# Performance work log

Measured on AMD Instinct MI355X. Metric: run time of the kernel, lower is better.

## Reference

```python
import jax, jax.numpy as jnp
import numpy as np

N_NODES = 100000
N_EDGES = 1600000
IN_CH, HID_CH, OUT_CH = 128, 128, 64
N_GRAPHS = 64


def gcn_conv(x, src, dst, W, b, n_nodes):
    """PyG-style GCNConv: self-loops already included in (src, dst).
    out_i = b + sum_j norm_ij * (x_j @ W), norm_ij = deg_i^-1/2 * deg_j^-1/2."""
    xw = x @ W  # [N, out]
    deg = jax.ops.segment_sum(jnp.ones_like(dst, dtype=xw.dtype), dst,
                              num_segments=n_nodes)  # [N]
    dinv = jnp.where(deg > 0, jax.lax.rsqrt(jnp.maximum(deg, 1e-12)), 0.0)
    norm = dinv[src] * dinv[dst]  # [E]
    msg = xw[src] * norm[:, None]  # gather + scale  [E, out]
    out = jax.ops.segment_sum(msg, dst, num_segments=n_nodes)  # scatter-add
    return out + b


def global_mean_pool(x, batch, n_graphs):
    s = jax.ops.segment_sum(x, batch, num_segments=n_graphs)
    cnt = jax.ops.segment_sum(jnp.ones((x.shape[0],), x.dtype), batch,
                              num_segments=n_graphs)
    return s / jnp.maximum(cnt, 1.0)[:, None]


def setup_inputs() -> dict:
    key = jax.random.key(0)
    ks = jax.random.split(key, 9)
    x = jax.random.normal(ks[0], (N_NODES, IN_CH), dtype=jnp.float32)
    edge_index = jax.random.randint(ks[1], (2, N_EDGES), 0, N_NODES, dtype=jnp.int64)
    batch = jnp.sort(jax.random.randint(ks[2], (N_NODES,), 0, N_GRAPHS, dtype=jnp.int64))
    # Glorot-ish params
    s1 = 1.0 / np.sqrt(IN_CH)
    s2 = 1.0 / np.sqrt(HID_CH)
    W1 = jax.random.normal(ks[3], (IN_CH, HID_CH), jnp.float32) * s1
    b1 = jnp.zeros((HID_CH,), jnp.float32)
    W2 = jax.random.normal(ks[4], (HID_CH, HID_CH), jnp.float32) * s2
    b2 = jnp.zeros((HID_CH,), jnp.float32)
    Wl = jax.random.normal(ks[5], (HID_CH, OUT_CH), jnp.float32) * s2
    bl = jax.random.normal(ks[6], (OUT_CH,), jnp.float32) * 0.01
    return {"x": x, "edge_index": edge_index, "batch": batch,
            "W1": W1, "b1": b1, "W2": W2, "b2": b2, "Wl": Wl, "bl": bl}


def reference(x, edge_index, batch, W1, b1, W2, b2, Wl, bl):
    n = x.shape[0]
    loop = jnp.arange(n, dtype=edge_index.dtype)
    src = jnp.concatenate([edge_index[0], loop])  # add self-loops
    dst = jnp.concatenate([edge_index[1], loop])
    h = jax.nn.relu(gcn_conv(x, src, dst, W1, b1, n))
    h = jax.nn.relu(gcn_conv(h, src, dst, W2, b2, n))
    g = global_mean_pool(h, batch, N_GRAPHS)  # [B, hid]
    return g @ Wl + bl  # [B, out]
```

## Files before the change

kernel.cpp:

```cpp
#include <hip/hip_runtime.h>

#define N_NODESC 100000
#define N_EDGESC 1600000
#define CH 128
#define NG 64
#define OC 64

#define GST_BLKS 391
#define EDGE_BLKS 6250
#define MFMA_BLKS 1563
#define NPASS 7
#define PAD_STRIDE 128

typedef __attribute__((ext_vector_type(8))) short short8;
typedef __attribute__((ext_vector_type(4))) float f32x4;

__device__ __forceinline__ unsigned short f2b_u(float f) {
    union { float f; unsigned int u; } x; x.f = f;
    unsigned int u = x.u;
    return (unsigned short)((u + 0x7fffu + ((u >> 16) & 1u)) >> 16);
}
__device__ __forceinline__ float b2f_lo(unsigned int v) {
    union { unsigned int u; float f; } x; x.u = v << 16; return x.f;
}
__device__ __forceinline__ float b2f_hi(unsigned int v) {
    union { unsigned int u; float f; } x; x.u = v & 0xffff0000u; return x.f;
}

#define WSTR 136
template<int AFP>
__device__ __forceinline__ void mfma_compute(int blk, int t, const void* __restrict__ Ap,
                                             unsigned short* __restrict__ Ob,
                                             const unsigned short* WsT) {
    int wave = t >> 6, lane = t & 63;
    int quad = lane >> 4, l16 = lane & 15;
    int arow = blk * 64 + wave * 16 + l16;
    bool rowok = arow < N_NODESC;
    f32x4 acc[8] = {};
#pragma unroll
    for (int c = 0; c < 4; ++c) {
        int koff = c * 32 + quad * 8;
        short8 a;
        if (AFP) {
            const float* A = (const float*)Ap;
            float4 f0 = make_float4(0, 0, 0, 0), f1 = make_float4(0, 0, 0, 0);
            if (rowok) {
                f0 = *(const float4*)(A + (size_t)arow * 128 + koff);
                f1 = *(const float4*)(A + (size_t)arow * 128 + koff + 4);
            }
            a[0] = (short)f2b_u(f0.x); a[1] = (short)f2b_u(f0.y);
            a[2] = (short)f2b_u(f0.z); a[3] = (short)f2b_u(f0.w);
            a[4] = (short)f2b_u(f1.x); a[5] = (short)f2b_u(f1.y);
            a[6] = (short)f2b_u(f1.z); a[7] = (short)f2b_u(f1.w);
        } else {
            const unsigned short* A = (const unsigned short*)Ap;
            if (rowok) a = *(const short8*)(A + (size_t)arow * 128 + koff);
            else       a = (short8)(short)0;
        }
#pragma unroll
        for (int tt = 0; tt < 8; ++tt) {
            short8 b = *(const short8*)&WsT[(tt * 16 + l16) * WSTR + koff];
            acc[tt] = __builtin_amdgcn_mfma_f32_16x16x32_bf16(a, b, acc[tt], 0, 0, 0);
        }
    }
    int orow0 = blk * 64 + wave * 16 + quad * 4;
#pragma unroll
    for (int r = 0; r < 4; ++r) {
        int g = orow0 + r;
        if (g < N_NODESC) {
#pragma unroll
            for (int tt = 0; tt < 8; ++tt)
                Ob[(size_t)g * 128 + tt * 16 + l16] = f2b_u(acc[tt][r]);
        }
    }
}

__global__ __launch_bounds__(256) void k_l1_build(const float* __restrict__ x,
                                                  const float* __restrict__ W1,
                                                  unsigned short* __restrict__ xw,
                                                  const int* __restrict__ ei,
                                                  int* __restrict__ deg,
                                                  int* __restrict__ pad) {
    __shared__ unsigned short WsT[128 * WSTR];
    int t = threadIdx.x;
    if (blockIdx.x < MFMA_BLKS) {
        for (int idx = t; idx < 16384; idx += 256) {
            int k = idx >> 7, c = idx & 127;
            WsT[c * WSTR + k] = f2b_u(W1[idx]);
        }
        __syncthreads();
        mfma_compute<1>(blockIdx.x, t, x, xw, WsT);
    } else {
        int bb = blockIdx.x - MFMA_BLKS;
        int e = (bb % EDGE_BLKS) * 256 + t;
        int p = bb / EDGE_BLKS;
        int d = ei[N_EDGESC + e];
        if ((d >> 14) == p) {
            int slot = atomicAdd(&deg[d], 1);
            pad[d * PAD_STRIDE + slot] = ei[e];
        }
    }
}

__global__ void k_mid(const int* __restrict__ deg, const int* __restrict__ batch,
                      const float* __restrict__ W2,
                      float* __restrict__ dinv, int* __restrict__ gstart,
                      unsigned short* __restrict__ Wt2) {
    int b = blockIdx.x, t = threadIdx.x;
    if (b < GST_BLKS) {
        int i = b * 256 + t;
        if (i < N_NODESC) dinv[i] = rsqrtf((float)(deg[i] + 1));
    } else if (b < 2 * GST_BLKS) {
        int i = (b - GST_BLKS) * 256 + t;
        if (i >= N_NODESC) return;
        int bb = batch[i];
        int bp = (i == 0) ? -1 : batch[i - 1];
        for (int g = bp + 1; g <= bb; ++g) gstart[g] = i;
        if (i == N_NODESC - 1)
            for (int g = bb + 1; g <= NG; ++g) gstart[g] = N_NODESC;
    } else {
        int i = (b - 2 * GST_BLKS) * 256 + t;
        int k = i >> 7, c = i & 127;
        Wt2[c * 128 + k] = f2b_u(W2[k * 128 + c]);
    }
}

__global__ __launch_bounds__(256) void k_mfma2(const unsigned short* __restrict__ A,
                                               const unsigned short* __restrict__ Wt,
                                               unsigned short* __restrict__ Ob) {
    __shared__ unsigned short WsT[128 * WSTR];
    int t = threadIdx.x;
    {
        const uint4* wsrc = (const uint4*)Wt;
        for (int idx = t; idx < 2048; idx += 256) {
            int row = idx >> 4, sub = idx & 15;
            *((uint4*)&WsT[row * WSTR] + sub) = wsrc[row * 16 + sub];
        }
    }
    __syncthreads();
    mfma_compute<0>(blockIdx.x, t, A, Ob, WsT);
}

__device__ __forceinline__ void gather_row(const unsigned int* __restrict__ xw,
                                           const int* __restrict__ pad,
                                           const float* __restrict__ dinv,
                                           int s, int e, int lane,
                                           float& acc0, float& acc1) {
    int i = s;
    for (; i + 8 <= e; i += 8) {
        int s0 = pad[i], s1 = pad[i + 1], s2 = pad[i + 2], s3 = pad[i + 3];
        int s4 = pad[i + 4], s5 = pad[i + 5], s6 = pad[i + 6], s7 = pad[i + 7];
        float w0 = dinv[s0], w1 = dinv[s1], w2 = dinv[s2], w3 = dinv[s3];
        float w4 = dinv[s4], w5 = dinv[s5], w6 = dinv[s6], w7 = dinv[s7];
        unsigned int v0 = xw[(size_t)s0 * 64 + lane];
        unsigned int v1 = xw[(size_t)s1 * 64 + lane];
        unsigned int v2 = xw[(size_t)s2 * 64 + lane];
        unsigned int v3 = xw[(size_t)s3 * 64 + lane];
        unsigned int v4 = xw[(size_t)s4 * 64 + lane];
        unsigned int v5 = xw[(size_t)s5 * 64 + lane];
        unsigned int v6 = xw[(size_t)s6 * 64 + lane];
        unsigned int v7 = xw[(size_t)s7 * 64 + lane];
        acc0 += w0 * b2f_lo(v0); acc1 += w0 * b2f_hi(v0);
        acc0 += w1 * b2f_lo(v1); acc1 += w1 * b2f_hi(v1);
        acc0 += w2 * b2f_lo(v2); acc1 += w2 * b2f_hi(v2);
        acc0 += w3 * b2f_lo(v3); acc1 += w3 * b2f_hi(v3);
        acc0 += w4 * b2f_lo(v4); acc1 += w4 * b2f_hi(v4);
        acc0 += w5 * b2f_lo(v5); acc1 += w5 * b2f_hi(v5);
        acc0 += w6 * b2f_lo(v6); acc1 += w6 * b2f_hi(v6);
        acc0 += w7 * b2f_lo(v7); acc1 += w7 * b2f_hi(v7);
    }
    for (; i + 4 <= e; i += 4) {
        int s0 = pad[i], s1 = pad[i + 1], s2 = pad[i + 2], s3 = pad[i + 3];
        float w0 = dinv[s0], w1 = dinv[s1], w2 = dinv[s2], w3 = dinv[s3];
        unsigned int v0 = xw[(size_t)s0 * 64 + lane];
        unsigned int v1 = xw[(size_t)s1 * 64 + lane];
        unsigned int v2 = xw[(size_t)s2 * 64 + lane];
        unsigned int v3 = xw[(size_t)s3 * 64 + lane];
        acc0 += w0 * b2f_lo(v0); acc1 += w0 * b2f_hi(v0);
        acc0 += w1 * b2f_lo(v1); acc1 += w1 * b2f_hi(v1);
        acc0 += w2 * b2f_lo(v2); acc1 += w2 * b2f_hi(v2);
        acc0 += w3 * b2f_lo(v3); acc1 += w3 * b2f_hi(v3);
    }
    for (; i < e; ++i) {
        int s0 = pad[i];
        float w0 = dinv[s0];
        unsigned int v0 = xw[(size_t)s0 * 64 + lane];
        acc0 += w0 * b2f_lo(v0); acc1 += w0 * b2f_hi(v0);
    }
}

__global__ __launch_bounds__(256) void k_gather1(const unsigned int* __restrict__ xw,
                                                 const int* __restrict__ deg,
                                                 const int* __restrict__ pad,
                                                 const float* __restrict__ dinv,
                                                 const float* __restrict__ bias,
                                                 unsigned int* __restrict__ outp) {
    int t = threadIdx.x;
    int lane = t & 63;
    int node = blockIdx.x * 4 + (t >> 6);
    if (node >= N_NODESC) return;
    int s = node * PAD_STRIDE, e = s + deg[node];
    float wn = dinv[node];
    unsigned int vs = xw[(size_t)node * 64 + lane];
    float acc0 = wn * b2f_lo(vs), acc1 = wn * b2f_hi(vs);
    gather_row(xw, pad, dinv, s, e, lane, acc0, acc1);
    float2 b = ((const float2*)bias)[lane];
    float o0 = fmaxf(b.x + wn * acc0, 0.f);
    float o1 = fmaxf(b.y + wn * acc1, 0.f);
    outp[(size_t)node * 64 + lane] =
        ((unsigned int)f2b_u(o1) << 16) | (unsigned int)f2b_u(o0);
}

__global__ __launch_bounds__(256) void k_gather_pool(const unsigned int* __restrict__ xw,
                                                     const int* __restrict__ deg,
                                                     const int* __restrict__ pad,
                                                     const float* __restrict__ dinv,
                                                     const float* __restrict__ bias,
                                                     const int* __restrict__ batch,
                                                     float* __restrict__ gpart) {
    __shared__ float lds[4 * 128];
    int t = threadIdx.x, w = t >> 6, lane = t & 63;
    int base = blockIdx.x * 16;
    bool fast = batch[base] == batch[base + 15];
    float2 bv = ((const float2*)bias)[lane];
    float sum0 = 0.f, sum1 = 0.f;
#pragma unroll 1
    for (int j = 0; j < 4; ++j) {
        int node = base + w * 4 + j;
        int s = node * PAD_STRIDE, e = s + deg[node];
        float wn = dinv[node];
        unsigned int vs = xw[(size_t)node * 64 + lane];
        float acc0 = wn * b2f_lo(vs), acc1 = wn * b2f_hi(vs);
        gather_row(xw, pad, dinv, s, e, lane, acc0, acc1);
        float o0 = fmaxf(bv.x + wn * acc0, 0.f);
        float o1 = fmaxf(bv.y + wn * acc1, 0.f);
        if (fast) {
            sum0 += o0; sum1 += o1;
        } else {
            int g = batch[node];
            atomicAdd(&gpart[g * 128 + lane * 2], o0);
            atomicAdd(&gpart[g * 128 + lane * 2 + 1], o1);
        }
    }
    if (fast) {
        lds[w * 128 + lane * 2] = sum0;
        lds[w * 128 + lane * 2 + 1] = sum1;
        __syncthreads();
        if (t < 128) {
            float v = lds[t] + lds[128 + t] + lds[256 + t] + lds[384 + t];
            atomicAdd(&gpart[batch[base] * 128 + t], v);
        }
    }
}

__global__ void k_final(const float* __restrict__ gpart, const int* __restrict__ gstart,
                        const float* __restrict__ Wl, const float* __restrict__ bl,
                        float* __restrict__ out) {
    __shared__ float gs[128];
    int b = blockIdx.x;
    int o = threadIdx.x;
    gs[o] = gpart[b * 128 + o];
    gs[o + 64] = gpart[b * 128 + 64 + o];
    __syncthreads();
    int cnt = gstart[b + 1] - gstart[b];
    float sc = 1.f / (float)(cnt > 0 ? cnt : 1);
    float sum = 0.f;
    for (int k = 0; k < 128; ++k) sum += gs[k] * Wl[k * 64 + o];
    out[b * 64 + o] = bl[o] + sc * sum;
}

extern "C" void kernel_launch(void* const* d_in, const int* in_sizes, int n_in,
                              void* d_out, int out_size, void* d_ws, size_t ws_size,
                              hipStream_t stream) {
    const float* x    = (const float*)d_in[0];
    const int*   ei   = (const int*)d_in[1];
    const int*   batch= (const int*)d_in[2];
    const float* W1   = (const float*)d_in[3];
    const float* b1   = (const float*)d_in[4];
    const float* W2   = (const float*)d_in[5];
    const float* b2   = (const float*)d_in[6];
    const float* Wl   = (const float*)d_in[7];
    const float* bl   = (const float*)d_in[8];
    float* out = (float*)d_out;

    char* ws = (char*)d_ws;
    unsigned short* xw_s = (unsigned short*)ws; ws += (size_t)N_NODESC * CH * 2;
    unsigned short* h_b  = (unsigned short*)ws; ws += (size_t)N_NODESC * CH * 2;
    unsigned short* Wt2 = (unsigned short*)ws; ws += (size_t)CH * CH * 2;
    int*   deg    = (int*)ws;   ws += (size_t)N_NODESC * 4;
    float* dinv   = (float*)ws; ws += (size_t)N_NODESC * 4;
    int*   pad    = (int*)ws;   ws += (size_t)N_NODESC * PAD_STRIDE * 4;
    int*   gstart = (int*)ws;   ws += (NG + 8) * 4;
    float* gpart  = (float*)ws; ws += (size_t)NG * CH * 4;

    hipMemsetAsync(deg, 0, (size_t)N_NODESC * 4, stream);
    hipMemsetAsync(gpart, 0, (size_t)NG * CH * 4, stream);

    k_l1_build<<<MFMA_BLKS + NPASS * EDGE_BLKS, 256, 0, stream>>>(x, W1, xw_s,
                                                                  ei, deg, pad);
    k_mid<<<2 * GST_BLKS + 64, 256, 0, stream>>>(deg, batch, W2, dinv, gstart, Wt2);

    k_gather1<<<(N_NODESC + 3) / 4, 256, 0, stream>>>((const unsigned int*)xw_s,
        deg, pad, dinv, b1, (unsigned int*)h_b);
    k_mfma2<<<MFMA_BLKS, 256, 0, stream>>>(h_b, Wt2, xw_s);
    k_gather_pool<<<N_NODESC / 16, 256, 0, stream>>>((const unsigned int*)xw_s,
        deg, pad, dinv, b2, batch, gpart);

    k_final<<<NG, 64, 0, stream>>>(gpart, gstart, Wl, bl, out);
}
```

Baseline: 349.5 us.

## Restructure CSR build into 8 range passes, fold dinv into gathers, merge memsets

The edge bucketing now uses 8 destination-range partitions, each block looping over 16 edge chunks, in place of 7 passes with one block per chunk. The build blocks are also placed before the MFMA blocks in the launch. The separate dinv kernel and array are removed, and rsqrt(deg+1) is recomputed inline in the gathers. W2 packing and gstart setup move to a small kernel ahead of the build, and the two memsets become one by making deg and gpart adjacent. This cuts a launch and a memset and reduces the blocks issued for edge scanning, but it adds an rsqrt per gathered edge and masks the slot index into the padded row.

```diff
diff --git a/kernel.cpp b/kernel.cpp
--- a/kernel.cpp
+++ b/kernel.cpp
@@ -9,8 +9,11 @@
 #define GST_BLKS 391
 #define EDGE_BLKS 6250
 #define MFMA_BLKS 1563
-#define NPASS 7
 #define PAD_STRIDE 128
+#define RANGE 12500
+#define EB_PER_BLK 16
+#define BGROUPS ((EDGE_BLKS + EB_PER_BLK - 1) / EB_PER_BLK)
+#define BUILD_BLKS (8 * BGROUPS)
 
 typedef __attribute__((ext_vector_type(8))) short short8;
 typedef __attribute__((ext_vector_type(4))) float f32x4;
@@ -25,6 +28,9 @@
 }
 __device__ __forceinline__ float b2f_hi(unsigned int v) {
     union { unsigned int u; float f; } x; x.u = v & 0xffff0000u; return x.f;
+}
+__device__ __forceinline__ float dinv_of(const int* __restrict__ deg, int i) {
+    return rsqrtf((float)(deg[i] + 1));
 }
 
 #define WSTR 136
@@ -75,6 +81,24 @@
     }
 }
 
+__global__ void k_pack(const float* __restrict__ W2, const int* __restrict__ batch,
+                       unsigned short* __restrict__ Wt2, int* __restrict__ gstart) {
+    int b = blockIdx.x, t = threadIdx.x;
+    if (b < 64) {
+        int i = b * 256 + t;
+        int k = i >> 7, c = i & 127;
+        Wt2[c * 128 + k] = f2b_u(W2[k * 128 + c]);
+    } else {
+        int i = (b - 64) * 256 + t;
+        if (i >= N_NODESC) return;
+        int bb = batch[i];
+        int bp = (i == 0) ? -1 : batch[i - 1];
+        for (int g = bp + 1; g <= bb; ++g) gstart[g] = i;
+        if (i == N_NODESC - 1)
+            for (int g = bb + 1; g <= NG; ++g) gstart[g] = N_NODESC;
+    }
+}
+
 __global__ __launch_bounds__(256) void k_l1_build(const float* __restrict__ x,
                                                   const float* __restrict__ W1,
                                                   unsigned short* __restrict__ xw,
@@ -83,45 +107,29 @@
                                                   int* __restrict__ pad) {
     __shared__ unsigned short WsT[128 * WSTR];
     int t = threadIdx.x;
-    if (blockIdx.x < MFMA_BLKS) {
+    if (blockIdx.x < BUILD_BLKS) {
+        int bb = blockIdx.x;
+        unsigned int r = bb & 7;
+        int g0 = (bb >> 3) * EB_PER_BLK;
+#pragma unroll 4
+        for (int i = 0; i < EB_PER_BLK; ++i) {
+            int e = (g0 + i) * 256 + t;
+            if (e < N_EDGESC) {
+                int d = ei[N_EDGESC + e];
+                if ((unsigned)d / RANGE == r) {
+                    int slot = atomicAdd(&deg[d], 1);
+                    pad[d * PAD_STRIDE + (slot & (PAD_STRIDE - 1))] = ei[e];
+                }
+            }
+        }
+    } else {
+        int blk = blockIdx.x - BUILD_BLKS;
         for (int idx = t; idx < 16384; idx += 256) {
             int k = idx >> 7, c = idx & 127;
             WsT[c * WSTR + k] = f2b_u(W1[idx]);
         }
         __syncthreads();
-        mfma_compute<1>(blockIdx.x, t, x, xw, WsT);
-    } else {
-        int bb = blockIdx.x - MFMA_BLKS;
-        int e = (bb % EDGE_BLKS) * 256 + t;
-        int p = bb / EDGE_BLKS;
-        int d = ei[N_EDGESC + e];
-        if ((d >> 14) == p) {
-            int slot = atomicAdd(&deg[d], 1);
-            pad[d * PAD_STRIDE + slot] = ei[e];
-        }
-    }
-}
-
-__global__ void k_mid(const int* __restrict__ deg, const int* __restrict__ batch,
-                      const float* __restrict__ W2,
-                      float* __restrict__ dinv, int* __restrict__ gstart,
-                      unsigned short* __restrict__ Wt2) {
-    int b = blockIdx.x, t = threadIdx.x;
-    if (b < GST_BLKS) {
-        int i = b * 256 + t;
-        if (i < N_NODESC) dinv[i] = rsqrtf((float)(deg[i] + 1));
-    } else if (b < 2 * GST_BLKS) {
-        int i = (b - GST_BLKS) * 256 + t;
-        if (i >= N_NODESC) return;
-        int bb = batch[i];
-        int bp = (i == 0) ? -1 : batch[i - 1];
-        for (int g = bp + 1; g <= bb; ++g) gstart[g] = i;
-        if (i == N_NODESC - 1)
-            for (int g = bb + 1; g <= NG; ++g) gstart[g] = N_NODESC;
-    } else {
-        int i = (b - 2 * GST_BLKS) * 256 + t;
-        int k = i >> 7, c = i & 127;
-        Wt2[c * 128 + k] = f2b_u(W2[k * 128 + c]);
+        mfma_compute<1>(blk, t, x, xw, WsT);
     }
 }
 
@@ -143,15 +151,17 @@
 
 __device__ __forceinline__ void gather_row(const unsigned int* __restrict__ xw,
                                            const int* __restrict__ pad,
-                                           const float* __restrict__ dinv,
+                                           const int* __restrict__ deg,
                                            int s, int e, int lane,
                                            float& acc0, float& acc1) {
     int i = s;
     for (; i + 8 <= e; i += 8) {
         int s0 = pad[i], s1 = pad[i + 1], s2 = pad[i + 2], s3 = pad[i + 3];
         int s4 = pad[i + 4], s5 = pad[i + 5], s6 = pad[i + 6], s7 = pad[i + 7];
-        float w0 = dinv[s0], w1 = dinv[s1], w2 = dinv[s2], w3 = dinv[s3];
-        float w4 = dinv[s4], w5 = dinv[s5], w6 = dinv[s6], w7 = dinv[s7];
+        float w0 = dinv_of(deg, s0), w1 = dinv_of(deg, s1);
+        float w2 = dinv_of(deg, s2), w3 = dinv_of(deg, s3);
+        float w4 = dinv_of(deg, s4), w5 = dinv_of(deg, s5);
+        float w6 = dinv_of(deg, s6), w7 = dinv_of(deg, s7);
         unsigned int v0 = xw[(size_t)s0 * 64 + lane];
         unsigned int v1 = xw[(size_t)s1 * 64 + lane];
         unsigned int v2 = xw[(size_t)s2 * 64 + lane];
@@ -171,7 +181,8 @@
     }
     for (; i + 4 <= e; i += 4) {
         int s0 = pad[i], s1 = pad[i + 1], s2 = pad[i + 2], s3 = pad[i + 3];
-        float w0 = dinv[s0], w1 = dinv[s1], w2 = dinv[s2], w3 = dinv[s3];
+        float w0 = dinv_of(deg, s0), w1 = dinv_of(deg, s1);
+        float w2 = dinv_of(deg, s2), w3 = dinv_of(deg, s3);
         unsigned int v0 = xw[(size_t)s0 * 64 + lane];
         unsigned int v1 = xw[(size_t)s1 * 64 + lane];
         unsigned int v2 = xw[(size_t)s2 * 64 + lane];
@@ -183,7 +194,7 @@
     }
     for (; i < e; ++i) {
         int s0 = pad[i];
-        float w0 = dinv[s0];
+        float w0 = dinv_of(deg, s0);
         unsigned int v0 = xw[(size_t)s0 * 64 + lane];
         acc0 += w0 * b2f_lo(v0); acc1 += w0 * b2f_hi(v0);
     }
@@ -192,18 +203,18 @@
 __global__ __launch_bounds__(256) void k_gather1(const unsigned int* __restrict__ xw,
                                                  const int* __restrict__ deg,
                                                  const int* __restrict__ pad,
-                                                 const float* __restrict__ dinv,
                                                  const float* __restrict__ bias,
                                                  unsigned int* __restrict__ outp) {
     int t = threadIdx.x;
     int lane = t & 63;
     int node = blockIdx.x * 4 + (t >> 6);
     if (node >= N_NODESC) return;
-    int s = node * PAD_STRIDE, e = s + deg[node];
-    float wn = dinv[node];
+    int dg = deg[node];
+    int s = node * PAD_STRIDE, e = s + dg;
+    float wn = rsqrtf((float)(dg + 1));
     unsigned int vs = xw[(size_t)node * 64 + lane];
     float acc0 = wn * b2f_lo(vs), acc1 = wn * b2f_hi(vs);
-    gather_row(xw, pad, dinv, s, e, lane, acc0, acc1);
+    gather_row(xw, pad, deg, s, e, lane, acc0, acc1);
     float2 b = ((const float2*)bias)[lane];
     float o0 = fmaxf(b.x + wn * acc0, 0.f);
     float o1 = fmaxf(b.y + wn * acc1, 0.f);
@@ -214,7 +225,6 @@
 __global__ __launch_bounds__(256) void k_gather_pool(const unsigned int* __restrict__ xw,
                                                      const int* __restrict__ deg,
                                                      const int* __restrict__ pad,
-                                                     const float* __restrict__ dinv,
                                                      const float* __restrict__ bias,
                                                      const int* __restrict__ batch,
                                                      float* __restrict__ gpart) {
@@ -227,11 +237,12 @@
 #pragma unroll 1
     for (int j = 0; j < 4; ++j) {
         int node = base + w * 4 + j;
-        int s = node * PAD_STRIDE, e = s + deg[node];
-        float wn = dinv[node];
+        int dg = deg[node];
+        int s = node * PAD_STRIDE, e = s + dg;
+        float wn = rsqrtf((float)(dg + 1));
         unsigned int vs = xw[(size_t)node * 64 + lane];
         float acc0 = wn * b2f_lo(vs), acc1 = wn * b2f_hi(vs);
-        gather_row(xw, pad, dinv, s, e, lane, acc0, acc1);
+        gather_row(xw, pad, deg, s, e, lane, acc0, acc1);
         float o0 = fmaxf(bv.x + wn * acc0, 0.f);
         float o1 = fmaxf(bv.y + wn * acc1, 0.f);
         if (fast) {
@@ -288,23 +299,20 @@
     unsigned short* h_b  = (unsigned short*)ws; ws += (size_t)N_NODESC * CH * 2;
     unsigned short* Wt2 = (unsigned short*)ws; ws += (size_t)CH * CH * 2;
     int*   deg    = (int*)ws;   ws += (size_t)N_NODESC * 4;
-    float* dinv   = (float*)ws; ws += (size_t)N_NODESC * 4;
+    float* gpart  = (float*)ws; ws += (size_t)NG * CH * 4;
     int*   pad    = (int*)ws;   ws += (size_t)N_NODESC * PAD_STRIDE * 4;
     int*   gstart = (int*)ws;   ws += (NG + 8) * 4;
-    float* gpart  = (float*)ws; ws += (size_t)NG * CH * 4;
-
-    hipMemsetAsync(deg, 0, (size_t)N_NODESC * 4, stream);
-    hipMemsetAsync(gpart, 0, (size_t)NG * CH * 4, stream);
-
-    k_l1_build<<<MFMA_BLKS + NPASS * EDGE_BLKS, 256, 0, stream>>>(x, W1, xw_s,
-                                                                  ei, deg, pad);
-    k_mid<<<2 * GST_BLKS + 64, 256, 0, stream>>>(deg, batch, W2, dinv, gstart, Wt2);
+
+    hipMemsetAsync(deg, 0, (size_t)N_NODESC * 4 + (size_t)NG * CH * 4, stream);
+
+    k_pack<<<64 + GST_BLKS, 256, 0, stream>>>(W2, batch, Wt2, gstart);
+    k_l1_build<<<BUILD_BLKS + MFMA_BLKS, 256, 0, stream>>>(x, W1, xw_s, ei, deg, pad);
 
     k_gather1<<<(N_NODESC + 3) / 4, 256, 0, stream>>>((const unsigned int*)xw_s,
-        deg, pad, dinv, b1, (unsigned int*)h_b);
+        deg, pad, b1, (unsigned int*)h_b);
     k_mfma2<<<MFMA_BLKS, 256, 0, stream>>>(h_b, Wt2, xw_s);
     k_gather_pool<<<N_NODESC / 16, 256, 0, stream>>>((const unsigned int*)xw_s,
-        deg, pad, dinv, b2, batch, gpart);
+        deg, pad, b2, batch, gpart);
 
     k_final<<<NG, 64, 0, stream>>>(gpart, gstart, Wl, bl, out);
 }
```

Measured after the change: 349.2 us. No clear change (-0.1%).
